# Performance work log

Hardware: AMD Instinct MI355X
Metric: run time of the kernel (lower is better)

The kernel has to match this reference:

```python
import jax, jax.numpy as jnp
import numpy as np

# Module configuration (from init_kwargs)
N, C_IN, C_OUT, L, V, P = 4, 64, 64, 1024, 25, 3
KERNEL_SIZE, STRIDE = 9, 1
EPS = 1e-5


def _toeplitz(length):
    # Faithful to: sum_i pad(eye(L - stride*i), (i*stride, 0, 0, i*stride))
    # -> ones at [r, r + i*stride] for i in range(kernel_size // stride)
    t = jnp.zeros((length, length), dtype=jnp.float32)
    for i in range(KERNEL_SIZE // STRIDE):  # small fixed loop over taps
        t = t + jnp.eye(length, k=i * STRIDE, dtype=jnp.float32)
    return t


def setup_inputs() -> dict:
    key = jax.random.key(0)
    k0, k1, k2, k3 = jax.random.split(key, 4)
    x = jax.random.normal(k0, (N, C_IN, L, V), dtype=jnp.float32)
    A = jax.random.uniform(k1, (P, V, V), dtype=jnp.float32)
    edge_importance = jnp.ones((P, V, V), dtype=jnp.float32)
    conv_w = jax.random.normal(k2, (C_OUT * P, C_IN, 1, 1), dtype=jnp.float32) * 0.05
    conv_b = jax.random.normal(k3, (C_OUT * P,), dtype=jnp.float32) * 0.05
    gamma = jnp.ones((C_OUT,), dtype=jnp.float32)
    beta = jnp.zeros((C_OUT,), dtype=jnp.float32)
    return {"x": x, "A": A, "edge_importance": edge_importance,
            "conv_w": conv_w, "conv_b": conv_b, "gamma": gamma, "beta": beta}


def reference(x, A, edge_importance, conv_w, conv_b, gamma, beta):
    n, _, l, v = x.shape
    res = x  # residual: in_channels == out_channels and stride == 1 -> identity

    # 1x1 conv: (N, C_in, L, V) -> (N, P*C_out, L, V)
    w = conv_w[:, :, 0, 0]  # (P*C_out, C_in)
    y = jnp.einsum('nclv,kc->nklv', x, w) + conv_b[None, :, None, None]

    # split into P chunks of C_out along channels, stack, permute -> (N, L, P, C_out, V)
    y = y.reshape(n, P, C_OUT, l, v).transpose(0, 3, 1, 2, 4)

    # partition-wise graph adjacency matmul with edge-importance mask
    y = jnp.einsum('nlpcv,pvw->nlpcw', y, A * edge_importance)

    # Toeplitz temporal conv: (N, P, C, V, L) @ (L, L)
    y = y.transpose(0, 2, 3, 4, 1)
    y = jnp.matmul(y, _toeplitz(l))
    y = y.sum(axis=1)            # sum over partitions -> (N, C, V, L)
    y = y.transpose(0, 1, 3, 2)  # (N, C, L, V)

    # BatchNorm2d with batch statistics (track_running_stats=False) + ReLU
    mean = y.mean(axis=(0, 2, 3), keepdims=True)
    var = y.var(axis=(0, 2, 3), keepdims=True)  # biased, as torch uses for normalization
    y = (y - mean) * jax.lax.rsqrt(var + EPS)
    y = y * gamma[None, :, None, None] + beta[None, :, None, None]
    y = jax.nn.relu(y)

    # do = Sequential(ReLU, Dropout(0.0)) applied to (y + res)
    return jax.nn.relu(y + res)
```

## Files before the change

### kernel.cpp

```cpp
#include <hip/hip_runtime.h>


typedef unsigned short ushort_t;
typedef __attribute__((ext_vector_type(8))) short short8;
typedef __attribute__((ext_vector_type(4))) float f32x4;
typedef __attribute__((ext_vector_type(4))) unsigned short us4;
typedef __attribute__((ext_vector_type(8))) unsigned short us8;

#define N_  4
#define CI_ 64
#define CO_ 64
#define L_  1024
#define V_  25
#define P_  3
#define KS_ 9
#define NLV 102400.0f
#define NREP 128

__device__ __forceinline__ float b2f(ushort_t u) {
  union { float f; unsigned int i; } c; c.i = ((unsigned int)u) << 16; return c.f;
}
__device__ __forceinline__ ushort_t f2b(float f) {
  union { float f; unsigned int i; } c; c.f = f;
  unsigned int u = c.i;
  u += 0x7fffu + ((u >> 16) & 1u);
  return (ushort_t)(u >> 16);
}

__global__ __launch_bounds__(256) void kwin(
    const float* __restrict__ x, ushort_t* __restrict__ xs,
    const float* __restrict__ A, const float* __restrict__ E,
    const float* __restrict__ cb, const float* __restrict__ W,
    ushort_t* __restrict__ a2raw, float* __restrict__ biastab,
    ushort_t* __restrict__ wb, float* __restrict__ statsbuf)
{
  const int chunk = blockIdx.x;
  const int n = blockIdx.y;
  const int tid = threadIdx.x;

  if (chunk == 128) {
    if (n != 0) return;
    __shared__ float colA[P_ * 32];
    if (tid < P_ * 32) {
      int p = tid >> 5, w = tid & 31;
      float s = 0.f;
      if (w < V_)
        for (int v = 0; v < V_; ++v) {
          int idx = (p * V_ + v) * V_ + w;
          s += A[idx] * E[idx];
        }
      colA[tid] = s;
    }
    for (int e = tid; e < 32 * 96; e += 256) {
      int w = e / 96, k = e - w * 96;
      int p = k >> 5, v = k & 31;
      float val = 0.f;
      if (w < V_ && v < V_) {
        int idx = (p * V_ + v) * V_ + w;
        val = A[idx] * E[idx];
      }
      a2raw[e] = f2b(val);
    }
    for (int e = tid; e < 192 * 64; e += 256) wb[e] = f2b(W[e]);
    __syncthreads();
    for (int e = tid; e < 32 * 64; e += 256) {
      int w = e >> 6, c = e & 63;
      float s = 0.f;
      for (int p = 0; p < P_; ++p) s += cb[p * 64 + c] * colA[p * 32 + w];
      biastab[e] = s;
    }
    for (int e = tid; e < NREP * 128; e += 256) statsbuf[e] = 0.f;
    return;
  }

  __shared__ ushort_t tile[64 * 402];
  const int l0 = chunk * 8;
  const long xn = (long)n * CI_ * L_ * V_;
  for (int m = tid; m < 6400; m += 256) {
    int ci = m / 100;
    int j4 = (m - ci * 100) * 4;
    f32x4 d;
    if (chunk == 0 && j4 < 200) {
      d = (f32x4){0.f, 0.f, 0.f, 0.f};
    } else {
      d = *(const f32x4*)(x + xn + (long)ci * (L_ * V_) + (l0 - 8) * V_ + j4);
    }
    ushort_t* dst = &tile[ci * 402 + j4];
    dst[0] = f2b(d[0]); dst[1] = f2b(d[1]); dst[2] = f2b(d[2]); dst[3] = f2b(d[3]);
  }
  __syncthreads();
  const long xsbase = ((long)n * L_ + l0) * 1600;
  for (int cid = tid; cid < 1600; cid += 256) {
    const int v = cid >> 6, ci = cid & 63;
    const ushort_t* col = &tile[ci * 402 + v];
    float s = 0.f;
#pragma unroll
    for (int li = 0; li < 9; ++li) s += b2f(col[li * 25]);
    xs[xsbase + cid] = f2b(s);
#pragma unroll
    for (int l_ = 1; l_ < 8; ++l_) {
      s += b2f(col[(l_ + 8) * 25]) - b2f(col[(l_ - 1) * 25]);
      xs[xsbase + l_ * 1600 + cid] = f2b(s);
    }
  }
}

__global__ __launch_bounds__(256) void kmain(
    const ushort_t* __restrict__ xs,
    const ushort_t* __restrict__ Wb,
    const ushort_t* __restrict__ a2,
    const float*    __restrict__ biastab,
    ushort_t*       __restrict__ zb,
    float*          __restrict__ statsbuf)
{
  const int lb = blockIdx.x;
  const int n  = blockIdx.y;
  const int tid = threadIdx.x, lane = tid & 63, wv = tid >> 6;
  const int m16 = lane & 15, quad = lane >> 4;

  __shared__ __align__(16) ushort_t XT[2 * 32 * 72];
  __shared__ __align__(16) ushort_t T1[2 * 64 * 104];

  {
    const ushort_t* src = xs + ((long)n * L_ + 2 * lb) * 1600;
    for (int m = tid; m < 400; m += 256) {
      int l_ = m / 200, mr = m - l_ * 200;
      int v = mr >> 3, sub = mr & 7;
      *(us8*)(&XT[l_ * 2304 + v * 72 + sub * 8]) = *(const us8*)(src + m * 8);
    }
    if (tid < 126) {
      int l_ = tid / 63, j = tid - l_ * 63;
      *(us8*)(&XT[l_ * 2304 + 1800 + j * 8]) = (us8){0,0,0,0,0,0,0,0};
    }
  }
  __syncthreads();

  short8 bfr[4][2];
#pragma unroll
  for (int nt = 0; nt < 4; ++nt)
#pragma unroll
    for (int ks = 0; ks < 2; ++ks)
      bfr[nt][ks] = *(const short8*)(
          &XT[(nt >> 1) * 2304 + ((nt & 1) * 16 + m16) * 72 + ks * 32 + quad * 8]);

  f32x4 acc1[3][4];
#pragma unroll
  for (int i = 0; i < 3; ++i)
#pragma unroll
    for (int j = 0; j < 4; ++j) acc1[i][j] = (f32x4){0.f, 0.f, 0.f, 0.f};

#pragma unroll
  for (int i = 0; i < 3; ++i) {
    const int mt = wv * 3 + i;
    const ushort_t* wrow = Wb + (mt * 16 + m16) * 64 + quad * 8;
    short8 af0 = *(const short8*)(wrow);
    short8 af1 = *(const short8*)(wrow + 32);
#pragma unroll
    for (int nt = 0; nt < 4; ++nt) {
      acc1[i][nt] = __builtin_amdgcn_mfma_f32_16x16x32_bf16(af0, bfr[nt][0], acc1[i][nt], 0, 0, 0);
      acc1[i][nt] = __builtin_amdgcn_mfma_f32_16x16x32_bf16(af1, bfr[nt][1], acc1[i][nt], 0, 0, 0);
    }
  }
#pragma unroll
  for (int i = 0; i < 3; ++i) {
    const int mt = wv * 3 + i;
#pragma unroll
    for (int nt = 0; nt < 4; ++nt) {
      const int l_ = nt >> 1;
      const int col = (nt & 1) * 16 + m16;
#pragma unroll
      for (int r = 0; r < 4; ++r) {
        int k = mt * 16 + quad * 4 + r;
        T1[l_ * 6656 + (k & 63) * 104 + (k >> 6) * 32 + col] = f2b(acc1[i][nt][r]);
      }
    }
  }
  __syncthreads();

  short8 bfr2[2][3];
#pragma unroll
  for (int nt = 0; nt < 2; ++nt)
#pragma unroll
    for (int ks = 0; ks < 3; ++ks)
      bfr2[nt][ks] = *(const short8*)(a2 + (nt * 16 + m16) * 96 + ks * 32 + quad * 8);

  f32x4 acc2[2][2];
#pragma unroll
  for (int l_ = 0; l_ < 2; ++l_)
#pragma unroll
    for (int nt = 0; nt < 2; ++nt) acc2[l_][nt] = (f32x4){0.f, 0.f, 0.f, 0.f};

#pragma unroll
  for (int l_ = 0; l_ < 2; ++l_) {
#pragma unroll
    for (int ks = 0; ks < 3; ++ks) {
      short8 af = *(const short8*)(&T1[l_ * 6656 + (wv * 16 + m16) * 104 + ks * 32 + quad * 8]);
      acc2[l_][0] = __builtin_amdgcn_mfma_f32_16x16x32_bf16(af, bfr2[0][ks], acc2[l_][0], 0, 0, 0);
      acc2[l_][1] = __builtin_amdgcn_mfma_f32_16x16x32_bf16(af, bfr2[1][ks], acc2[l_][1], 0, 0, 0);
    }
  }

  const int cbase = wv * 16 + quad * 4;
  float s1[4] = {0.f, 0.f, 0.f, 0.f}, s2[4] = {0.f, 0.f, 0.f, 0.f};
#pragma unroll
  for (int l_ = 0; l_ < 2; ++l_) {
    const int l = 2 * lb + l_;
    const float cnt = (float)(l + 1 < KS_ ? l + 1 : KS_);
#pragma unroll
    for (int nt = 0; nt < 2; ++nt) {
      const int w = nt * 16 + m16;
      if (w < V_) {
        f32x4 bias = *(const f32x4*)(biastab + w * 64 + cbase);
        us4 pack;
#pragma unroll
        for (int r = 0; r < 4; ++r) {
          pack[r] = f2b(acc2[l_][nt][r] + cnt * bias[r]);
          float zr = b2f(pack[r]);
          s1[r] += zr; s2[r] += zr * zr;
        }
        *(us4*)(&zb[(((long)(n * L_ + l) * V_ + w) << 6) + cbase]) = pack;
      }
    }
  }
#pragma unroll
  for (int off = 1; off < 16; off <<= 1) {
#pragma unroll
    for (int r = 0; r < 4; ++r) {
      s1[r] += __shfl_xor(s1[r], off, 64);
      s2[r] += __shfl_xor(s2[r], off, 64);
    }
  }
  if (m16 == 0) {
    float* sb = statsbuf + ((n * 512 + lb) & (NREP - 1)) * 128;
#pragma unroll
    for (int r = 0; r < 4; ++r) {
      atomicAdd(&sb[cbase + r], s1[r]);
      atomicAdd(&sb[64 + cbase + r], s2[r]);
    }
  }
}

__global__ __launch_bounds__(256) void kapply(
    const ushort_t* __restrict__ zb, const float* __restrict__ x,
    const float* __restrict__ statsbuf,
    const float* __restrict__ gamma, const float* __restrict__ beta,
    float* __restrict__ out)
{
  const int n = blockIdx.y, chunk = blockIdx.x;
  const int tid = threadIdx.x;
  __shared__ ushort_t zl[100 * 66];
  __shared__ float red[4][64][2];
  __shared__ float sc[64], sh[64];
  const long zbase = (long)((n * L_ + chunk * 4) * V_) * 64;
  for (int m = tid; m < 3200; m += 256) {
    int rr = m >> 5, c2 = (m & 31) * 2;
    *(unsigned int*)(&zl[rr * 66 + c2]) = ((const unsigned int*)(zb + zbase))[m];
  }
  {
    const int c = tid & 63, grp = tid >> 6;
    float a = 0.f, b = 0.f;
    for (int k = grp; k < NREP; k += 4) {
      a += statsbuf[k * 128 + c];
      b += statsbuf[k * 128 + 64 + c];
    }
    red[grp][c][0] = a;
    red[grp][c][1] = b;
  }
  __syncthreads();
  if (tid < 64) {
    const float inv = 1.0f / NLV;
    float s  = red[0][tid][0] + red[1][tid][0] + red[2][tid][0] + red[3][tid][0];
    float sq = red[0][tid][1] + red[1][tid][1] + red[2][tid][1] + red[3][tid][1];
    float mean = s * inv;
    float var  = sq * inv - mean * mean;
    float rstd = rsqrtf(var + 1e-5f);
    float g = gamma[tid];
    sc[tid] = rstd * g;
    sh[tid] = beta[tid] - mean * rstd * g;
  }
  __syncthreads();
  for (int e = tid; e < 6400; e += 256) {
    int c = e / 100, rr = e - c * 100;
    float z = b2f(zl[rr * 66 + c]);
    float y = fmaxf(z * sc[c] + sh[c], 0.f);
    long xi = ((long)(n * 64 + c) * L_ + chunk * 4) * V_ + rr;
    float o = fmaxf(y + x[xi], 0.f);
    out[xi] = o;
  }
}

extern "C" void kernel_launch(void* const* d_in, const int* in_sizes, int n_in,
                              void* d_out, int out_size, void* d_ws, size_t ws_size,
                              hipStream_t stream)
{
  const float* x     = (const float*)d_in[0];
  const float* A     = (const float*)d_in[1];
  const float* E     = (const float*)d_in[2];
  const float* W     = (const float*)d_in[3];
  const float* cb    = (const float*)d_in[4];
  const float* gamma = (const float*)d_in[5];
  const float* beta  = (const float*)d_in[6];
  float* out = (float*)d_out;

  char* ws = (char*)d_ws;
  const size_t XS_OFF   = 0;
  const size_t ZB_OFF   = 13107200;
  const size_t WB_OFF   = 26214400;
  const size_t A2_OFF   = WB_OFF + 32768;
  const size_t BIAS_OFF = A2_OFF + 16384;
  const size_t STAT_OFF = BIAS_OFF + 16384;
  ushort_t* xs      = (ushort_t*)(ws + XS_OFF);
  ushort_t* zb      = (ushort_t*)(ws + ZB_OFF);
  ushort_t* wb      = (ushort_t*)(ws + WB_OFF);
  ushort_t* a2      = (ushort_t*)(ws + A2_OFF);
  float*    biastab = (float*)(ws + BIAS_OFF);
  float*    statsbuf= (float*)(ws + STAT_OFF);

  kwin  <<<dim3(129, N_), 256, 0, stream>>>(x, xs, A, E, cb, W, a2, biastab, wb, statsbuf);
  kmain <<<dim3(512, N_), 256, 0, stream>>>(xs, wb, a2, biastab, zb, statsbuf);
  kapply<<<dim3(256, N_), 256, 0, stream>>>(zb, x, statsbuf, gamma, beta, out);
}
```

Baseline: 136.9 us.

## Store intermediate in NCLV layout so apply kernel streams vectorized without LDS transpose

The main kernel now writes the bf16 intermediate directly in the output's (N, C, L, V) layout using scalar 2-byte stores instead of packed channel-last 8-byte stores. The apply kernel then reads z, x and writes out with contiguous 16-element vector accesses and one channel per thread, dropping the shared-memory transpose, and launches a flat 1600-block grid. The cost moves into kmain, whose stores become scattered 2-byte writes strided by L*V across channels, which may hurt write coalescing there.

```diff
diff --git a/kernel.cpp b/kernel.cpp
--- a/kernel.cpp
+++ b/kernel.cpp
@@ -4,7 +4,6 @@
 typedef unsigned short ushort_t;
 typedef __attribute__((ext_vector_type(8))) short short8;
 typedef __attribute__((ext_vector_type(4))) float f32x4;
-typedef __attribute__((ext_vector_type(4))) unsigned short us4;
 typedef __attribute__((ext_vector_type(8))) unsigned short us8;
 
 #define N_  4
@@ -211,14 +210,13 @@
       const int w = nt * 16 + m16;
       if (w < V_) {
         f32x4 bias = *(const f32x4*)(biastab + w * 64 + cbase);
-        us4 pack;
 #pragma unroll
         for (int r = 0; r < 4; ++r) {
-          pack[r] = f2b(acc2[l_][nt][r] + cnt * bias[r]);
-          float zr = b2f(pack[r]);
+          ushort_t pv = f2b(acc2[l_][nt][r] + cnt * bias[r]);
+          float zr = b2f(pv);
           s1[r] += zr; s2[r] += zr * zr;
+          zb[((long)((n * 64 + cbase + r) * L_) + l) * V_ + w] = pv;
         }
-        *(us4*)(&zb[(((long)(n * L_ + l) * V_ + w) << 6) + cbase]) = pack;
       }
     }
   }
@@ -246,16 +244,9 @@
     const float* __restrict__ gamma, const float* __restrict__ beta,
     float* __restrict__ out)
 {
-  const int n = blockIdx.y, chunk = blockIdx.x;
   const int tid = threadIdx.x;
-  __shared__ ushort_t zl[100 * 66];
   __shared__ float red[4][64][2];
   __shared__ float sc[64], sh[64];
-  const long zbase = (long)((n * L_ + chunk * 4) * V_) * 64;
-  for (int m = tid; m < 3200; m += 256) {
-    int rr = m >> 5, c2 = (m & 31) * 2;
-    *(unsigned int*)(&zl[rr * 66 + c2]) = ((const unsigned int*)(zb + zbase))[m];
-  }
   {
     const int c = tid & 63, grp = tid >> 6;
     float a = 0.f, b = 0.f;
@@ -279,13 +270,22 @@
     sh[tid] = beta[tid] - mean * rstd * g;
   }
   __syncthreads();
-  for (int e = tid; e < 6400; e += 256) {
-    int c = e / 100, rr = e - c * 100;
-    float z = b2f(zl[rr * 66 + c]);
-    float y = fmaxf(z * sc[c] + sh[c], 0.f);
-    long xi = ((long)(n * 64 + c) * L_ + chunk * 4) * V_ + rr;
-    float o = fmaxf(y + x[xi], 0.f);
-    out[xi] = o;
+  const long base = ((long)blockIdx.x * 256 + tid) * 16;
+  const int c = (int)((base / 25600) & 63);
+  const float scc = sc[c], shc = sh[c];
+#pragma unroll
+  for (int h = 0; h < 2; ++h) {
+    us8 zp = *(const us8*)(zb + base + h * 8);
+    f32x4 xa = *(const f32x4*)(x + base + h * 8);
+    f32x4 xb = *(const f32x4*)(x + base + h * 8 + 4);
+    f32x4 oa, ob;
+#pragma unroll
+    for (int j = 0; j < 4; ++j) {
+      oa[j] = fmaxf(fmaxf(b2f(zp[j]) * scc + shc, 0.f) + xa[j], 0.f);
+      ob[j] = fmaxf(fmaxf(b2f(zp[4 + j]) * scc + shc, 0.f) + xb[j], 0.f);
+    }
+    *(f32x4*)(out + base + h * 8) = oa;
+    *(f32x4*)(out + base + h * 8 + 4) = ob;
   }
 }
 
@@ -318,5 +318,5 @@
 
   kwin  <<<dim3(129, N_), 256, 0, stream>>>(x, xs, A, E, cb, W, a2, biastab, wb, statsbuf);
   kmain <<<dim3(512, N_), 256, 0, stream>>>(xs, wb, a2, biastab, zb, statsbuf);
-  kapply<<<dim3(256, N_), 256, 0, stream>>>(zb, x, statsbuf, gamma, beta, out);
-}
+  kapply<<<1600, 256, 0, stream>>>(zb, x, statsbuf, gamma, beta, out);
+}
```

Result: no change. 138.1 us (+0.9%).
